# Optimization experiments

Measured on AMD Instinct MI355X. Metric: run time of the kernel, lower is better.

## Reference

```python
import jax, jax.numpy as jnp
import numpy as np
import math

B, IC, OC, WDIM, RES, K = 16, 512, 512, 512, 64, 3
LRELU_GAIN = math.sqrt(2.0)  # bias_act def_gain for lrelu


def setup_inputs() -> dict:
    key = jax.random.key(0)
    ks = jax.random.split(key, 8)
    return {
        "x": jax.random.normal(ks[0], (B, IC, RES, RES), dtype=jnp.float32),
        "w": jax.random.normal(ks[1], (B, WDIM), dtype=jnp.float32),
        "conv_weight": jax.random.normal(ks[2], (OC, IC, K, K), dtype=jnp.float32),
        "affine_weight": jax.random.normal(ks[3], (IC, WDIM), dtype=jnp.float32),
        "affine_bias": jnp.ones((IC,), dtype=jnp.float32),  # bias_init=1
        "bias": jax.random.normal(ks[4], (OC,), dtype=jnp.float32) * 0.1,
        "noise_const": jax.random.normal(ks[5], (RES, RES), dtype=jnp.float32),
        "noise_strength": jax.random.normal(ks[6], (), dtype=jnp.float32) * 0.1,
    }


def reference(x, w, conv_weight, affine_weight, affine_bias, bias, noise_const, noise_strength):
    # affine: styles = w @ (W * 1/sqrt(w_dim)).T + b  (linear activation, bias_gain=1)
    weight_gain = 1.0 / math.sqrt(WDIM)
    styles = w @ (affine_weight * weight_gain).T + affine_bias  # [B, IC]

    # modulate + demodulate per-sample weights
    wm = conv_weight[None] * styles[:, None, :, None, None]          # [B,OC,IC,K,K]
    dcoefs = jax.lax.rsqrt(jnp.sum(wm * wm, axis=(2, 3, 4)) + 1e-8)  # [B,OC]
    wm = wm * dcoefs[:, :, None, None, None]

    # grouped conv (groups=batch) == per-sample conv; up=1 -> flip_weight=True -> cross-correlation
    pad = K // 2
    def conv1(xi, wi):
        return jax.lax.conv_general_dilated(
            xi[None], wi, window_strides=(1, 1), padding=[(pad, pad), (pad, pad)],
            dimension_numbers=("NCHW", "OIHW", "NCHW"))[0]
    y = jax.vmap(conv1)(x, wm)  # [B,OC,RES,RES]

    # const noise, then fused bias + lrelu(0.2) * sqrt(2), no clamp
    y = y + noise_const * noise_strength
    y = y + bias[None, :, None, None]
    y = jnp.where(y >= 0, y, 0.2 * y) * jnp.asarray(LRELU_GAIN, y.dtype)
    return y
```

## Files before the change

### kernel.cpp

```cpp
#include <hip/hip_runtime.h>
#include <hip/hip_bf16.h>
#include <cstdint>

#define B_    16
#define IC_   512
#define OC_   512
#define RES_  64
#define WDIM_ 512
#define HW_   4096

#define XROWS 10
#define XCOLS 66
#define XsEL (XROWS * XCOLS * 32)

typedef __attribute__((ext_vector_type(8))) short short8;
typedef __attribute__((ext_vector_type(4))) float f32x4;
typedef __attribute__((address_space(3))) unsigned int lds_uint;
typedef const __attribute__((address_space(1))) unsigned int g_uint;

__device__ __forceinline__ unsigned int f2bf_bits(float f) {
    unsigned int x = __builtin_bit_cast(unsigned int, f);
    x += 0x7fffu + ((x >> 16) & 1u);
    return x >> 16;
}

__global__ __launch_bounds__(256) void k_styles(const float* __restrict__ w,
        const float* __restrict__ aw, const float* __restrict__ ab,
        float* __restrict__ styles) {
    int bx = blockIdx.x;
    int b = bx >> 7;
    int wave = threadIdx.x >> 6, lane = threadIdx.x & 63;
    int ic = ((bx & 127) << 2) + wave;
    const float* wr = w + b * WDIM_;
    const float* awr = aw + ic * WDIM_;
    float s = 0.f;
    #pragma unroll
    for (int j = 0; j < 8; ++j) {
        int k = lane + (j << 6);
        s += wr[k] * awr[k];
    }
    #pragma unroll
    for (int off = 32; off > 0; off >>= 1) s += __shfl_down(s, off);
    if (lane == 0) styles[b * IC_ + ic] = s * 0.044194173824159216f + ab[ic];
}

__global__ __launch_bounds__(256) void k_wprep(const float* __restrict__ cw,
        float* __restrict__ S2, unsigned short* __restrict__ wbf) {
    int gid = blockIdx.x * 256 + threadIdx.x;
    int oc = gid >> 9, ic = gid & 511;
    const float* p = cw + gid * 9;
    float v[9]; float ss = 0.f;
    #pragma unroll
    for (int t = 0; t < 9; ++t) { v[t] = p[t]; ss += v[t] * v[t]; }
    S2[gid] = ss;
    int chunk = ic >> 5;
    int base = (chunk * 512 + oc) * 32 + (ic & 31);
    #pragma unroll
    for (int t = 0; t < 9; ++t)
        wbf[t * (16 * 512 * 32) + base] = (unsigned short)f2bf_bits(v[t]);
}

__global__ __launch_bounds__(256) void k_xprep(const float* __restrict__ x,
        const float* __restrict__ styles, unsigned short* __restrict__ xpack) {
    unsigned int flat = blockIdx.x * 256 + threadIdx.x;
    int gp  = flat & 3;
    int col = (flat >> 2) & 63;
    int row = (flat >> 8) & 63;
    int c   = (flat >> 14) & 15;
    int b   = flat >> 18;
    int swz = ((col + 1) >> 1) & 3;
    int ic0 = c * 32 + 8 * (gp ^ swz);
    const float* xp = x + (size_t)(b * IC_ + ic0) * HW_ + row * RES_ + col;
    const float* st = styles + b * IC_ + ic0;
    unsigned int o[4];
    #pragma unroll
    for (int h = 0; h < 4; ++h) {
        float a0 = xp[(size_t)(2 * h) * HW_]     * st[2 * h];
        float a1 = xp[(size_t)(2 * h + 1) * HW_] * st[2 * h + 1];
        o[h] = f2bf_bits(a0) | (f2bf_bits(a1) << 16);
    }
    uint4* dst = (uint4*)(xpack + (size_t)flat * 8);
    *dst = make_uint4(o[0], o[1], o[2], o[3]);
}

__global__ __launch_bounds__(256) void k_dcoef(const float* __restrict__ styles,
        const float* __restrict__ S2, float* __restrict__ dcoefs) {
    int bx = blockIdx.x;
    int b = bx >> 7;
    int wave = threadIdx.x >> 6, lane = threadIdx.x & 63;
    int oc = ((bx & 127) << 2) + wave;
    const float* st = styles + b * IC_;
    const float* s2 = S2 + oc * IC_;
    float s = 0.f;
    #pragma unroll
    for (int j = 0; j < 8; ++j) {
        int k = lane + (j << 6);
        float a = st[k];
        s += a * a * s2[k];
    }
    #pragma unroll
    for (int off = 32; off > 0; off >>= 1) s += __shfl_down(s, off);
    if (lane == 0) dcoefs[b * OC_ + oc] = rsqrtf(s + 1e-8f);
}

__global__ __launch_bounds__(512, 2) void k_conv(
        const unsigned short* __restrict__ xpack,
        const float* __restrict__ dcoefs, const unsigned short* __restrict__ wbf,
        const float* __restrict__ bias, const float* __restrict__ noise,
        const float* __restrict__ nstr, float* __restrict__ out) {

    __shared__ __align__(16) unsigned short Xs[2 * XsEL + 2048];

    const int tid = threadIdx.x;
    const int lane = tid & 63;
    const int wave = tid >> 6;
    const int lane15 = lane & 15, kg = lane >> 4;
    const int wm = wave >> 2, wn = wave & 3;
    const int nt = blockIdx.x, oct = blockIdx.y, b = blockIdx.z;
    const int oc0 = oct * 128, r0 = nt * 8;

    const unsigned short* xpk = xpack + (size_t)b * (16 * 64 * 2048);

    const int dhalf = tid >> 8;
    const int doff  = tid & 255;
    auto dma_chunk = [&](int c, int buf) {
        unsigned short* XbW = Xs + buf * XsEL;
        #pragma unroll
        for (int r = 0; r < 5; ++r) {
            int rl = r * 2 + dhalf;
            int grow = r0 - 1 + rl;
            bool ok = (grow >= 0) && (grow < RES_);
            int gsrc = ok ? grow : (grow < 0 ? 0 : RES_ - 1);
            const unsigned short* src =
                xpk + ((size_t)((c << 6) + gsrc) << 11) + (doff << 3);
            unsigned short* ldst = ok
                ? (XbW + ((rl * XCOLS + 1) << 5) + (doff << 3))
                : (Xs + 2 * XsEL + (doff << 3));
            __builtin_amdgcn_global_load_lds((g_uint*)src, (lds_uint*)ldst,
                                             16, 0, 0);
        }
    };

    const unsigned short* wlane =
        wbf + (size_t)(oc0 + wm * 64 + lane15) * 32 + (kg << 3);
    auto loadA = [&](int c2, int t2, short8* dst) {
        const unsigned short* g = wlane + (size_t)(t2 * 16 + c2) * (512 * 32);
        #pragma unroll
        for (int mf = 0; mf < 4; ++mf)
            dst[mf] = *(const short8*)(g + (mf << 9));
    };

    {
        unsigned int* xz = (unsigned int*)Xs;
        for (int i = tid; i < XsEL + 1024; i += 512) xz[i] = 0u;
    }
    __syncthreads();
    dma_chunk(0, 0);
    __syncthreads();

    f32x4 acc[4][8];
    #pragma unroll
    for (int mf = 0; mf < 4; ++mf)
        #pragma unroll
        for (int nf = 0; nf < 8; ++nf)
            acc[mf][nf] = (f32x4){0.f, 0.f, 0.f, 0.f};

    for (int c = 0; c < 16; ++c) {
        const unsigned short* Xb = Xs + (c & 1) * XsEL;
        short8 afc[4];
        loadA(c, 0, afc);
        #pragma unroll
        for (int t = 0; t < 9; ++t) {
            short8 afn[4];
            if (t < 8) loadA(c, t + 1, afn);
            if (t == 2 && c < 15) dma_chunk(c + 1, (c + 1) & 1);
            const int kh = t / 3, kw = t % 3;
            short8 bfr[8];
            #pragma unroll
            for (int nf = 0; nf < 8; ++nf) {
                int rl = (wn << 1) + (nf >> 2) + kh;
                int cl = ((nf & 3) << 4) + lane15 + kw;
                int gp = kg ^ ((cl >> 1) & 3);
                int el = (rl * XCOLS + cl) * 32 + (gp << 3);
                bfr[nf] = *(const short8*)(Xb + el);
            }
            #pragma unroll
            for (int mf = 0; mf < 4; ++mf)
                #pragma unroll
                for (int nf = 0; nf < 8; ++nf)
                    acc[mf][nf] = __builtin_amdgcn_mfma_f32_16x16x32_bf16(
                        afc[mf], bfr[nf], acc[mf][nf], 0, 0, 0);
            if (t < 8) {
                #pragma unroll
                for (int mf = 0; mf < 4; ++mf) afc[mf] = afn[mf];
            }
        }
        __syncthreads();
    }

    const float nstrength = nstr[0];
    float* outb = out + (size_t)(b * OC_ + oc0) * HW_ + nt * (8 * RES_);
    float nz[8];
    #pragma unroll
    for (int nf = 0; nf < 8; ++nf) {
        int n = (wn << 7) + (nf << 4) + lane15;
        nz[nf] = noise[nt * 512 + n] * nstrength;
    }
    #pragma unroll
    for (int mf = 0; mf < 4; ++mf) {
        #pragma unroll
        for (int r = 0; r < 4; ++r) {
            int ocl = wm * 64 + (mf << 4) + (kg << 2) + r;
            float dc = dcoefs[b * OC_ + oc0 + ocl];
            float bv = bias[oc0 + ocl];
            #pragma unroll
            for (int nf = 0; nf < 8; ++nf) {
                int n = (wn << 7) + (nf << 4) + lane15;
                float vv = acc[mf][nf][r] * dc + nz[nf] + bv;
                vv = (vv >= 0.f ? vv : 0.2f * vv) * 1.4142135623730951f;
                outb[(size_t)ocl * HW_ + n] = vv;
            }
        }
    }
}

extern "C" void kernel_launch(void* const* d_in, const int* in_sizes, int n_in,
                              void* d_out, int out_size, void* d_ws, size_t ws_size,
                              hipStream_t stream) {
    const float* x     = (const float*)d_in[0];
    const float* w     = (const float*)d_in[1];
    const float* cw    = (const float*)d_in[2];
    const float* aw    = (const float*)d_in[3];
    const float* ab    = (const float*)d_in[4];
    const float* bias  = (const float*)d_in[5];
    const float* noise = (const float*)d_in[6];
    const float* nstr  = (const float*)d_in[7];
    float* out = (float*)d_out;

    uint8_t* ws = (uint8_t*)d_ws;
    float* styles = (float*)ws;
    float* dcoefs = (float*)(ws + 32768);
    float* S2     = (float*)(ws + 65536);
    unsigned short* wbf   = (unsigned short*)(ws + 65536 + 1048576);
    unsigned short* xpack = (unsigned short*)(ws + 8388608);

    hipLaunchKernelGGL(k_styles, dim3(2048), dim3(256), 0, stream, w, aw, ab, styles);
    hipLaunchKernelGGL(k_xprep,  dim3(16384), dim3(256), 0, stream, x, styles, xpack);
    hipLaunchKernelGGL(k_wprep,  dim3(1024), dim3(256), 0, stream, cw, S2, wbf);
    hipLaunchKernelGGL(k_dcoef,  dim3(2048), dim3(256), 0, stream, styles, S2, dcoefs);
    hipLaunchKernelGGL(k_conv, dim3(8, 4, 16), dim3(512), 0, stream,
                       xpack, dcoefs, wbf, bias, noise, nstr, out);
}
```

Before: 756.5 us.

## Shrink conv tile to 64 OC by 4 rows with 256-thread blocks

The conv block tile shrinks from 128 output channels by 8 rows with 8 waves to 64 channels by 4 rows with 4 waves. The grid is flattened to 2048 blocks ordered batch and row-tile first within each channel group. The per-block LDS footprint and accumulators get smaller so more blocks can be resident per CU, and the A-fragment prefetch now runs across chunk boundaries. In exchange each block reuses less data: halo rows are a larger fraction of the X tile and weights are reloaded by more blocks, which raises global and L2 traffic.

```diff
diff --git a/kernel.cpp b/kernel.cpp
--- a/kernel.cpp
+++ b/kernel.cpp
@@ -9,9 +9,9 @@
 #define WDIM_ 512
 #define HW_   4096
 
-#define XROWS 10
+#define XR6   6
 #define XCOLS 66
-#define XsEL (XROWS * XCOLS * 32)
+#define XsEL6 (XR6 * XCOLS * 32)
 
 typedef __attribute__((ext_vector_type(8))) short short8;
 typedef __attribute__((ext_vector_type(4))) float f32x4;
@@ -103,46 +103,45 @@
     if (lane == 0) dcoefs[b * OC_ + oc] = rsqrtf(s + 1e-8f);
 }
 
-__global__ __launch_bounds__(512, 2) void k_conv(
+__global__ __launch_bounds__(256, 3) void k_conv(
         const unsigned short* __restrict__ xpack,
         const float* __restrict__ dcoefs, const unsigned short* __restrict__ wbf,
         const float* __restrict__ bias, const float* __restrict__ noise,
         const float* __restrict__ nstr, float* __restrict__ out) {
 
-    __shared__ __align__(16) unsigned short Xs[2 * XsEL + 2048];
+    __shared__ __align__(16) unsigned short Xs[2 * XsEL6 + 512];
 
     const int tid = threadIdx.x;
     const int lane = tid & 63;
-    const int wave = tid >> 6;
+    const int wn = tid >> 6;
     const int lane15 = lane & 15, kg = lane >> 4;
-    const int wm = wave >> 2, wn = wave & 3;
-    const int nt = blockIdx.x, oct = blockIdx.y, b = blockIdx.z;
-    const int oc0 = oct * 128, r0 = nt * 8;
+    const int bid = blockIdx.x;
+    const int oct = bid >> 8;
+    const int kk  = bid & 255;
+    const int nt  = kk & 15;
+    const int b   = kk >> 4;
+    const int oc0 = oct * 64, r0 = nt * 4;
 
     const unsigned short* xpk = xpack + (size_t)b * (16 * 64 * 2048);
 
-    const int dhalf = tid >> 8;
-    const int doff  = tid & 255;
     auto dma_chunk = [&](int c, int buf) {
-        unsigned short* XbW = Xs + buf * XsEL;
-        #pragma unroll
-        for (int r = 0; r < 5; ++r) {
-            int rl = r * 2 + dhalf;
-            int grow = r0 - 1 + rl;
+        unsigned short* XbW = Xs + buf * XsEL6;
+        #pragma unroll
+        for (int r = 0; r < 6; ++r) {
+            int grow = r0 - 1 + r;
             bool ok = (grow >= 0) && (grow < RES_);
-            int gsrc = ok ? grow : (grow < 0 ? 0 : RES_ - 1);
+            int gsrc = ok ? grow : 0;
             const unsigned short* src =
-                xpk + ((size_t)((c << 6) + gsrc) << 11) + (doff << 3);
+                xpk + ((size_t)((c << 6) + gsrc) << 11) + (tid << 3);
             unsigned short* ldst = ok
-                ? (XbW + ((rl * XCOLS + 1) << 5) + (doff << 3))
-                : (Xs + 2 * XsEL + (doff << 3));
+                ? (XbW + ((r * XCOLS + 1) << 5) + (tid << 3))
+                : (Xs + 2 * XsEL6 + (lane << 3));
             __builtin_amdgcn_global_load_lds((g_uint*)src, (lds_uint*)ldst,
                                              16, 0, 0);
         }
     };
 
-    const unsigned short* wlane =
-        wbf + (size_t)(oc0 + wm * 64 + lane15) * 32 + (kg << 3);
+    const unsigned short* wlane = wbf + (size_t)(oc0 + lane15) * 32 + (kg << 3);
     auto loadA = [&](int c2, int t2, short8* dst) {
         const unsigned short* g = wlane + (size_t)(t2 * 16 + c2) * (512 * 32);
         #pragma unroll
@@ -152,70 +151,70 @@
 
     {
         unsigned int* xz = (unsigned int*)Xs;
-        for (int i = tid; i < XsEL + 1024; i += 512) xz[i] = 0u;
+        for (int i = tid; i < XsEL6 + 256; i += 256) xz[i] = 0u;
     }
     __syncthreads();
     dma_chunk(0, 0);
     __syncthreads();
 
-    f32x4 acc[4][8];
+    f32x4 acc[4][4];
     #pragma unroll
     for (int mf = 0; mf < 4; ++mf)
         #pragma unroll
-        for (int nf = 0; nf < 8; ++nf)
+        for (int nf = 0; nf < 4; ++nf)
             acc[mf][nf] = (f32x4){0.f, 0.f, 0.f, 0.f};
 
+    short8 afc[4];
+    loadA(0, 0, afc);
+
     for (int c = 0; c < 16; ++c) {
-        const unsigned short* Xb = Xs + (c & 1) * XsEL;
-        short8 afc[4];
-        loadA(c, 0, afc);
+        const unsigned short* Xb = Xs + (c & 1) * XsEL6;
         #pragma unroll
         for (int t = 0; t < 9; ++t) {
             short8 afn[4];
-            if (t < 8) loadA(c, t + 1, afn);
+            {
+                int c2 = (t < 8) ? c : ((c + 1) & 15);
+                int t2 = (t < 8) ? (t + 1) : 0;
+                loadA(c2, t2, afn);
+            }
             if (t == 2 && c < 15) dma_chunk(c + 1, (c + 1) & 1);
             const int kh = t / 3, kw = t % 3;
-            short8 bfr[8];
-            #pragma unroll
-            for (int nf = 0; nf < 8; ++nf) {
-                int rl = (wn << 1) + (nf >> 2) + kh;
-                int cl = ((nf & 3) << 4) + lane15 + kw;
+            short8 bfr[4];
+            #pragma unroll
+            for (int nf = 0; nf < 4; ++nf) {
+                int cl = (nf << 4) + lane15 + kw;
                 int gp = kg ^ ((cl >> 1) & 3);
-                int el = (rl * XCOLS + cl) * 32 + (gp << 3);
+                int el = ((wn + kh) * XCOLS + cl) * 32 + (gp << 3);
                 bfr[nf] = *(const short8*)(Xb + el);
             }
             #pragma unroll
             for (int mf = 0; mf < 4; ++mf)
                 #pragma unroll
-                for (int nf = 0; nf < 8; ++nf)
+                for (int nf = 0; nf < 4; ++nf)
                     acc[mf][nf] = __builtin_amdgcn_mfma_f32_16x16x32_bf16(
                         afc[mf], bfr[nf], acc[mf][nf], 0, 0, 0);
-            if (t < 8) {
-                #pragma unroll
-                for (int mf = 0; mf < 4; ++mf) afc[mf] = afn[mf];
-            }
+            #pragma unroll
+            for (int mf = 0; mf < 4; ++mf) afc[mf] = afn[mf];
         }
         __syncthreads();
     }
 
     const float nstrength = nstr[0];
-    float* outb = out + (size_t)(b * OC_ + oc0) * HW_ + nt * (8 * RES_);
-    float nz[8];
-    #pragma unroll
-    for (int nf = 0; nf < 8; ++nf) {
-        int n = (wn << 7) + (nf << 4) + lane15;
-        nz[nf] = noise[nt * 512 + n] * nstrength;
-    }
+    float* outb = out + (size_t)(b * OC_ + oc0) * HW_ + (size_t)r0 * RES_;
+    float nz[4];
+    #pragma unroll
+    for (int nf = 0; nf < 4; ++nf)
+        nz[nf] = noise[(r0 + wn) * RES_ + (nf << 4) + lane15] * nstrength;
     #pragma unroll
     for (int mf = 0; mf < 4; ++mf) {
         #pragma unroll
         for (int r = 0; r < 4; ++r) {
-            int ocl = wm * 64 + (mf << 4) + (kg << 2) + r;
+            int ocl = (mf << 4) + (kg << 2) + r;
             float dc = dcoefs[b * OC_ + oc0 + ocl];
             float bv = bias[oc0 + ocl];
             #pragma unroll
-            for (int nf = 0; nf < 8; ++nf) {
-                int n = (wn << 7) + (nf << 4) + lane15;
+            for (int nf = 0; nf < 4; ++nf) {
+                int n = (wn << 6) + (nf << 4) + lane15;
                 float vv = acc[mf][nf][r] * dc + nz[nf] + bv;
                 vv = (vv >= 0.f ? vv : 0.2f * vv) * 1.4142135623730951f;
                 outb[(size_t)ocl * HW_ + n] = vv;
@@ -248,6 +247,6 @@
     hipLaunchKernelGGL(k_xprep,  dim3(16384), dim3(256), 0, stream, x, styles, xpack);
     hipLaunchKernelGGL(k_wprep,  dim3(1024), dim3(256), 0, stream, cw, S2, wbf);
     hipLaunchKernelGGL(k_dcoef,  dim3(2048), dim3(256), 0, stream, styles, S2, dcoefs);
-    hipLaunchKernelGGL(k_conv, dim3(8, 4, 16), dim3(512), 0, stream,
+    hipLaunchKernelGGL(k_conv, dim3(2048), dim3(256), 0, stream,
                        xpack, dcoefs, wbf, bias, noise, nstr, out);
 }
```

Result: faster. 662.6 us (-12.4%).
